# Optimization experiments

Hardware: AMD Instinct MI355X
Metric: run time of the kernel (lower is better)

## Reference

```python
import jax, jax.numpy as jnp
import numpy as np

B, T, D, H = 32, 4096, 512, 512


def setup_inputs() -> dict:
    key = jax.random.key(0)
    ks = jax.random.split(key, 8)
    s = 1.0 / np.sqrt(D)
    return {
        "hidden_state": jax.random.normal(ks[0], (B, D), jnp.float32),
        "encoder_outputs": jax.random.normal(ks[1], (B, T, D), jnp.float32),
        "W": jax.random.normal(ks[2], (D, H), jnp.float32) * s,
        "U": jax.random.normal(ks[3], (D, H), jnp.float32) * s,
        "V": jax.random.normal(ks[4], (H,), jnp.float32) * s,
        "bias": jnp.zeros((H,), jnp.float32),
        "Wa": jax.random.normal(ks[5], (H, H), jnp.float32) * (1.0 / np.sqrt(H)),
        "ba": jnp.zeros((H,), jnp.float32),
    }


def reference(hidden_state, encoder_outputs, W, U, V, bias, Wa, ba):
    # dens1: [B,1,H] ; dens2: [B,T,H]
    dens1 = jnp.einsum('bd,dh->bh', hidden_state, W)[:, None, :]
    dens2 = jnp.einsum('btd,dh->bth', encoder_outputs, U)
    pre = dens1 + dens2 + bias                       # [B,T,H]
    tanh_ = jnp.tanh(jnp.einsum('bth,hk->btk', pre, Wa) + ba)  # extra Dense(tanh)
    cij = jnp.einsum('bth,h->bt', tanh_, V)          # [B,T]
    alphas = jax.nn.softmax(cij, axis=-1)            # [B,T]
    output = jnp.einsum('btd,bt->bd', encoder_outputs, alphas)  # weighted sum
    return output, alphas
```

## Files before the change

### kernel.cpp

```cpp
#include <hip/hip_runtime.h>
#include <hip/hip_bf16.h>


#define BB 32
#define TT 4096
#define DD 512
#define HH 512
#define BK 64

typedef short s16x8 __attribute__((ext_vector_type(8)));
typedef float f32x4 __attribute__((ext_vector_type(4)));

union FU { float f; unsigned u; };

static __device__ __forceinline__ unsigned pack_bf16_trunc(float a, float b) {
    FU ua, ub; ua.f = a; ub.f = b;
    return (ua.u >> 16) | (ub.u & 0xffff0000u);
}

static __device__ __forceinline__ unsigned short f2bf_rne(float x) {
    FU v; v.f = x;
    unsigned u = v.u;
    u = u + 0x7fffu + ((u >> 16) & 1u);
    return (unsigned short)(u >> 16);
}

static __device__ __forceinline__ float tanh_fast(float x) {
    float e = __expf(2.0f * x);
    return 1.0f - 2.0f * __builtin_amdgcn_rcpf(e + 1.0f);
}

static __device__ __forceinline__ void gload_lds16(const void* g, void* l) {
    __builtin_amdgcn_global_load_lds(
        (const __attribute__((address_space(1))) unsigned int*)g,
        (__attribute__((address_space(3))) unsigned int*)l, 16, 0, 0);
}

__global__ void k_prep(const float* __restrict__ hs, const float* __restrict__ W,
                       const float* __restrict__ bias, const float* __restrict__ Wa,
                       const float* __restrict__ ba, const float* __restrict__ U,
                       float* __restrict__ cvec, unsigned short* __restrict__ UWaT) {
    int bi = blockIdx.x;
    int tid = threadIdx.x;
    __shared__ float sm[8 * DD];
    if (bi < 32) {
        int b = bi;
        float* hsb = sm;
        float* gs = sm + DD;
        hsb[tid] = hs[b * DD + tid];
        hsb[tid + 256] = hs[b * DD + tid + 256];
        __syncthreads();
        float a0 = bias[tid], a1 = bias[tid + 256];
        #pragma unroll 4
        for (int d = 0; d < DD; ++d) {
            float h = hsb[d];
            a0 = fmaf(h, W[(size_t)d * HH + tid], a0);
            a1 = fmaf(h, W[(size_t)d * HH + tid + 256], a1);
        }
        gs[tid] = a0;
        gs[tid + 256] = a1;
        __syncthreads();
        float c0 = ba[tid], c1 = ba[tid + 256];
        #pragma unroll 4
        for (int h = 0; h < HH; ++h) {
            float g = gs[h];
            c0 = fmaf(g, Wa[(size_t)h * HH + tid], c0);
            c1 = fmaf(g, Wa[(size_t)h * HH + tid + 256], c1);
        }
        cvec[b * HH + tid] = c0;
        cvec[b * HH + tid + 256] = c1;
    } else {
        int d0 = (bi - 32) * 8;
        float (*Us)[DD] = (float (*)[DD])sm;
        #pragma unroll
        for (int i = 0; i < 16; ++i) {
            int idx = i * 256 + tid;
            Us[idx >> 9][idx & 511] = U[(size_t)(d0 + (idx >> 9)) * HH + (idx & 511)];
        }
        __syncthreads();
        float acc[8][2] = {};
        #pragma unroll 2
        for (int h = 0; h < DD; ++h) {
            float w0 = Wa[(size_t)h * HH + tid];
            float w1 = Wa[(size_t)h * HH + 256 + tid];
            #pragma unroll
            for (int dd = 0; dd < 8; ++dd) {
                float u = Us[dd][h];
                acc[dd][0] = fmaf(u, w0, acc[dd][0]);
                acc[dd][1] = fmaf(u, w1, acc[dd][1]);
            }
        }
        #pragma unroll
        for (int dd = 0; dd < 8; ++dd) {
            UWaT[(size_t)tid * DD + d0 + dd] = f2bf_rne(acc[dd][0]);
            UWaT[(size_t)(tid + 256) * DD + d0 + dd] = f2bf_rne(acc[dd][1]);
        }
    }
}

__global__ void __launch_bounds__(256, 2) k_gemm_tanh(
    const float* __restrict__ e, const unsigned short* __restrict__ Bt,
    const float* __restrict__ cvec, const float* __restrict__ V,
    float* __restrict__ cij) {
    int tid = threadIdx.x;
    int m0 = blockIdx.x * 64;
    int lane = tid & 63, w = tid >> 6;
    int wn = w * 128;
    int lcol = lane & 15, q = lane >> 4;
    int rl = lane >> 3, gg = lane & 7;

    __shared__ __align__(16) unsigned short As[64 * BK];
    __shared__ __align__(16) unsigned short Bs[512 * BK];

    f32x4 acc[4][8] = {};

    int arow[4], ac4[4];
    #pragma unroll
    for (int it = 0; it < 4; ++it) {
        int idx = it * 256 + tid;
        arow[it] = idx >> 4;
        ac4[it] = idx & 15;
    }
    const float* Abase = e + (size_t)m0 * DD;

    float4 av[4];
    #pragma unroll
    for (int it = 0; it < 4; ++it)
        av[it] = *(const float4*)(Abase + (size_t)arow[it] * DD + ac4[it] * 4);

    for (int k0 = 0; k0 < DD; k0 += BK) {
        if (k0) __syncthreads();
        #pragma unroll
        for (int u = 0; u < 16; ++u) {
            int n0 = w * 128 + u * 8;
            const unsigned short* gp =
                Bt + (size_t)(n0 + rl) * DD + k0 + ((gg ^ rl) << 3);
            gload_lds16(gp, &Bs[n0 * 64]);
        }
        #pragma unroll
        for (int it = 0; it < 4; ++it) {
            uint2 wv;
            wv.x = pack_bf16_trunc(av[it].x, av[it].y);
            wv.y = pack_bf16_trunc(av[it].z, av[it].w);
            int g = ac4[it] >> 1, half = ac4[it] & 1;
            *(uint2*)&As[(g * 64 + (arow[it] ^ g)) * 8 + half * 4] = wv;
        }
        __syncthreads();
        if (k0 < DD - BK) {
            #pragma unroll
            for (int it = 0; it < 4; ++it)
                av[it] = *(const float4*)(Abase + (size_t)arow[it] * DD +
                                          (k0 + BK) + ac4[it] * 4);
        }
        #pragma unroll
        for (int ks = 0; ks < BK; ks += 32) {
            int gk = ks >> 3;
            s16x8 af[4], bfr[8];
            #pragma unroll
            for (int i = 0; i < 4; ++i) {
                int row = i * 16 + lcol, g = gk + q;
                af[i] = *(const s16x8*)&As[(g * 64 + (row ^ g)) * 8];
            }
            #pragma unroll
            for (int j = 0; j < 8; ++j) {
                int col = wn + j * 16 + lcol, g = gk + q;
                bfr[j] = *(const s16x8*)&Bs[col * 64 + ((g ^ (col & 7)) << 3)];
            }
            #pragma unroll
            for (int i = 0; i < 4; ++i)
                #pragma unroll
                for (int j = 0; j < 8; ++j)
                    acc[i][j] = __builtin_amdgcn_mfma_f32_16x16x32_bf16(
                        af[i], bfr[j], acc[i][j], 0, 0, 0);
        }
    }

    __syncthreads();
    float* red = (float*)As;
    int b = m0 >> 12;
    float cvv[8], Vv[8];
    #pragma unroll
    for (int j = 0; j < 8; ++j) {
        int h = wn + j * 16 + lcol;
        cvv[j] = cvec[b * HH + h];
        Vv[j] = V[h];
    }
    #pragma unroll
    for (int i = 0; i < 4; ++i) {
        #pragma unroll
        for (int r = 0; r < 4; ++r) {
            float s = 0.0f;
            #pragma unroll
            for (int j = 0; j < 8; ++j)
                s = fmaf(tanh_fast(acc[i][j][r] + cvv[j]), Vv[j], s);
            s += __shfl_xor(s, 1);
            s += __shfl_xor(s, 2);
            s += __shfl_xor(s, 4);
            s += __shfl_xor(s, 8);
            if (lcol == 0)
                red[w * 64 + i * 16 + q * 4 + r] = s;
        }
    }
    __syncthreads();
    if (tid < 64)
        cij[m0 + tid] = red[tid] + red[64 + tid] + red[128 + tid] + red[192 + tid];
}

__global__ void k_softmax(const float* __restrict__ cij, float* __restrict__ alphas) {
    int b = blockIdx.x, tid = threadIdx.x;
    const float* row = cij + (size_t)b * TT;
    __shared__ float red[4];
    float m = -1e30f;
    for (int t = tid; t < TT; t += 256) m = fmaxf(m, row[t]);
    #pragma unroll
    for (int o = 1; o < 64; o <<= 1) m = fmaxf(m, __shfl_xor(m, o));
    if ((tid & 63) == 0) red[tid >> 6] = m;
    __syncthreads();
    m = fmaxf(fmaxf(red[0], red[1]), fmaxf(red[2], red[3]));
    __syncthreads();
    float sum = 0.0f;
    for (int t = tid; t < TT; t += 256) sum += __expf(row[t] - m);
    #pragma unroll
    for (int o = 1; o < 64; o <<= 1) sum += __shfl_xor(sum, o);
    if ((tid & 63) == 0) red[tid >> 6] = sum;
    __syncthreads();
    float inv = 1.0f / (red[0] + red[1] + red[2] + red[3]);
    for (int t = tid; t < TT; t += 256)
        alphas[(size_t)b * TT + t] = __expf(row[t] - m) * inv;
}

__global__ void k_wsum(const float* __restrict__ e, const float* __restrict__ alphas,
                       float* __restrict__ pw) {
    int b = blockIdx.x >> 6;
    int chunk = blockIdx.x & 63;
    int tid = threadIdx.x;
    int half = tid >> 7, f4 = tid & 127;
    const float* base = e + (size_t)b * TT * DD + (size_t)chunk * 64 * DD + f4 * 4;
    const float* al = alphas + (size_t)b * TT + chunk * 64;
    f32x4 a0 = {0,0,0,0}, a1 = {0,0,0,0}, a2 = {0,0,0,0}, a3 = {0,0,0,0};
    for (int it = 0; it < 8; ++it) {
        int t = it * 8 + half;
        float w0 = al[t], w1 = al[t + 2], w2 = al[t + 4], w3 = al[t + 6];
        a0 += w0 * *(const f32x4*)(base + (size_t)t * DD);
        a1 += w1 * *(const f32x4*)(base + (size_t)(t + 2) * DD);
        a2 += w2 * *(const f32x4*)(base + (size_t)(t + 4) * DD);
        a3 += w3 * *(const f32x4*)(base + (size_t)(t + 6) * DD);
    }
    a0 += a1; a2 += a3; a0 += a2;
    __shared__ f32x4 red[128];
    if (half == 1) red[f4] = a0;
    __syncthreads();
    if (half == 0) {
        a0 += red[f4];
        *(f32x4*)&pw[((size_t)(b * 64 + chunk)) * DD + f4 * 4] = a0;
    }
}

__global__ void k_wred(const float* __restrict__ pw, float* __restrict__ out) {
    int b = blockIdx.x, tid = threadIdx.x;
    float2 acc = {0.0f, 0.0f};
    const float* base = pw + (size_t)b * 64 * DD;
    #pragma unroll 4
    for (int c = 0; c < 64; ++c) {
        float2 v = *(const float2*)(base + (size_t)c * DD + tid * 2);
        acc.x += v.x;
        acc.y += v.y;
    }
    *(float2*)&out[b * DD + tid * 2] = acc;
}

extern "C" void kernel_launch(void* const* d_in, const int* in_sizes, int n_in,
                              void* d_out, int out_size, void* d_ws, size_t ws_size,
                              hipStream_t stream) {
    const float* hs   = (const float*)d_in[0];
    const float* e    = (const float*)d_in[1];
    const float* W    = (const float*)d_in[2];
    const float* U    = (const float*)d_in[3];
    const float* V    = (const float*)d_in[4];
    const float* bias = (const float*)d_in[5];
    const float* Wa   = (const float*)d_in[6];
    const float* ba   = (const float*)d_in[7];

    float* out    = (float*)d_out;
    float* alphas = out + BB * DD;

    float*          cij  = (float*)d_ws;
    float*          cvec = (float*)((char*)d_ws + 524288);
    unsigned short* Bt   = (unsigned short*)((char*)d_ws + 589824);
    float*          pw   = (float*)((char*)d_ws + 1179648);


    k_prep<<<96, 256, 0, stream>>>(hs, W, bias, Wa, ba, U, cvec, Bt);
    k_gemm_tanh<<<2048, 256, 0, stream>>>(e, Bt, cvec, V, cij);
    k_softmax<<<BB, 256, 0, stream>>>(cij, alphas);
    k_wsum<<<BB * 64, 256, 0, stream>>>(e, alphas, pw);
    k_wred<<<BB, 256, 0, stream>>>(pw, out);
}
```

Before: 569.6 us.

## Pre-swizzle B into MFMA fragment layout and stage full A tile in LDS

The prep kernel now writes the fused U·Wa weight matrix in a fragment-major layout, so each lane of the GEMM kernel loads its B operand straight from global/L2 into registers with one 16-byte load. The B staging in LDS goes away, and those loads are double-buffered across the 16 k-steps. The whole 64x512 A tile is converted to bf16 and stored in LDS once up front, which removes the per-k-step barriers. In exchange, LDS use per block grows to 64KB for A and there is no prefetch of A overlapped with compute. The B operand is also re-read from L2 by every block instead of being shared through LDS.

```diff
diff --git a/kernel.cpp b/kernel.cpp
--- a/kernel.cpp
+++ b/kernel.cpp
@@ -6,7 +6,6 @@
 #define TT 4096
 #define DD 512
 #define HH 512
-#define BK 64
 
 typedef short s16x8 __attribute__((ext_vector_type(8)));
 typedef float f32x4 __attribute__((ext_vector_type(4)));
@@ -30,16 +29,10 @@
     return 1.0f - 2.0f * __builtin_amdgcn_rcpf(e + 1.0f);
 }
 
-static __device__ __forceinline__ void gload_lds16(const void* g, void* l) {
-    __builtin_amdgcn_global_load_lds(
-        (const __attribute__((address_space(1))) unsigned int*)g,
-        (__attribute__((address_space(3))) unsigned int*)l, 16, 0, 0);
-}
-
 __global__ void k_prep(const float* __restrict__ hs, const float* __restrict__ W,
                        const float* __restrict__ bias, const float* __restrict__ Wa,
                        const float* __restrict__ ba, const float* __restrict__ U,
-                       float* __restrict__ cvec, unsigned short* __restrict__ UWaT) {
+                       float* __restrict__ cvec, unsigned short* __restrict__ Btf) {
     int bi = blockIdx.x;
     int tid = threadIdx.x;
     __shared__ float sm[8 * DD];
@@ -90,16 +83,21 @@
                 acc[dd][1] = fmaf(u, w1, acc[dd][1]);
             }
         }
-        #pragma unroll
-        for (int dd = 0; dd < 8; ++dd) {
-            UWaT[(size_t)tid * DD + d0 + dd] = f2bf_rne(acc[dd][0]);
-            UWaT[(size_t)(tid + 256) * DD + d0 + dd] = f2bf_rne(acc[dd][1]);
+        int fk = d0 >> 5, qq = (d0 >> 3) & 3;
+        #pragma unroll
+        for (int half = 0; half < 2; ++half) {
+            int n = tid + half * 256;
+            unsigned short tmp[8];
+            #pragma unroll
+            for (int dd = 0; dd < 8; ++dd) tmp[dd] = f2bf_rne(acc[dd][half]);
+            size_t base = ((size_t)((n >> 4) * 16 + fk) * 64 + (n & 15) + (qq << 4)) * 8;
+            *(uint4*)&Btf[base] = *(const uint4*)tmp;
         }
     }
 }
 
 __global__ void __launch_bounds__(256, 2) k_gemm_tanh(
-    const float* __restrict__ e, const unsigned short* __restrict__ Bt,
+    const float* __restrict__ e, const unsigned short* __restrict__ Btf,
     const float* __restrict__ cvec, const float* __restrict__ V,
     float* __restrict__ cij) {
     int tid = threadIdx.x;
@@ -107,72 +105,54 @@
     int lane = tid & 63, w = tid >> 6;
     int wn = w * 128;
     int lcol = lane & 15, q = lane >> 4;
-    int rl = lane >> 3, gg = lane & 7;
-
-    __shared__ __align__(16) unsigned short As[64 * BK];
-    __shared__ __align__(16) unsigned short Bs[512 * BK];
-
+
+    __shared__ __align__(16) unsigned short As[64 * DD];
+
+    const float* Abase = e + (size_t)m0 * DD;
+    #pragma unroll
+    for (int it = 0; it < 16; ++it) {
+        int idx = it * 256 + tid;
+        int m = idx >> 6, c2 = idx & 63;
+        const float* p = Abase + (size_t)m * DD + c2 * 8;
+        float4 v0 = *(const float4*)p;
+        float4 v1 = *(const float4*)(p + 4);
+        uint4 u;
+        u.x = pack_bf16_trunc(v0.x, v0.y);
+        u.y = pack_bf16_trunc(v0.z, v0.w);
+        u.z = pack_bf16_trunc(v1.x, v1.y);
+        u.w = pack_bf16_trunc(v1.z, v1.w);
+        *(uint4*)&As[(m * 64 + (c2 ^ m)) * 8] = u;
+    }
+    __syncthreads();
+
+    const unsigned short* Bw = Btf + (size_t)(w * 8) * 16 * 64 * 8;
     f32x4 acc[4][8] = {};
-
-    int arow[4], ac4[4];
-    #pragma unroll
-    for (int it = 0; it < 4; ++it) {
-        int idx = it * 256 + tid;
-        arow[it] = idx >> 4;
-        ac4[it] = idx & 15;
-    }
-    const float* Abase = e + (size_t)m0 * DD;
-
-    float4 av[4];
-    #pragma unroll
-    for (int it = 0; it < 4; ++it)
-        av[it] = *(const float4*)(Abase + (size_t)arow[it] * DD + ac4[it] * 4);
-
-    for (int k0 = 0; k0 < DD; k0 += BK) {
-        if (k0) __syncthreads();
-        #pragma unroll
-        for (int u = 0; u < 16; ++u) {
-            int n0 = w * 128 + u * 8;
-            const unsigned short* gp =
-                Bt + (size_t)(n0 + rl) * DD + k0 + ((gg ^ rl) << 3);
-            gload_lds16(gp, &Bs[n0 * 64]);
-        }
-        #pragma unroll
-        for (int it = 0; it < 4; ++it) {
-            uint2 wv;
-            wv.x = pack_bf16_trunc(av[it].x, av[it].y);
-            wv.y = pack_bf16_trunc(av[it].z, av[it].w);
-            int g = ac4[it] >> 1, half = ac4[it] & 1;
-            *(uint2*)&As[(g * 64 + (arow[it] ^ g)) * 8 + half * 4] = wv;
-        }
-        __syncthreads();
-        if (k0 < DD - BK) {
-            #pragma unroll
-            for (int it = 0; it < 4; ++it)
-                av[it] = *(const float4*)(Abase + (size_t)arow[it] * DD +
-                                          (k0 + BK) + ac4[it] * 4);
-        }
-        #pragma unroll
-        for (int ks = 0; ks < BK; ks += 32) {
-            int gk = ks >> 3;
-            s16x8 af[4], bfr[8];
-            #pragma unroll
-            for (int i = 0; i < 4; ++i) {
-                int row = i * 16 + lcol, g = gk + q;
-                af[i] = *(const s16x8*)&As[(g * 64 + (row ^ g)) * 8];
-            }
-            #pragma unroll
-            for (int j = 0; j < 8; ++j) {
-                int col = wn + j * 16 + lcol, g = gk + q;
-                bfr[j] = *(const s16x8*)&Bs[col * 64 + ((g ^ (col & 7)) << 3)];
-            }
-            #pragma unroll
-            for (int i = 0; i < 4; ++i)
-                #pragma unroll
-                for (int j = 0; j < 8; ++j)
-                    acc[i][j] = __builtin_amdgcn_mfma_f32_16x16x32_bf16(
-                        af[i], bfr[j], acc[i][j], 0, 0, 0);
-        }
+    s16x8 bfr[2][8];
+    #pragma unroll
+    for (int j = 0; j < 8; ++j)
+        bfr[0][j] = *(const s16x8*)(Bw + ((size_t)(j * 16 + 0) * 64 + lane) * 8);
+
+    #pragma unroll
+    for (int kk = 0; kk < 16; ++kk) {
+        int cur = kk & 1;
+        if (kk < 15) {
+            #pragma unroll
+            for (int j = 0; j < 8; ++j)
+                bfr[cur ^ 1][j] =
+                    *(const s16x8*)(Bw + ((size_t)(j * 16 + kk + 1) * 64 + lane) * 8);
+        }
+        s16x8 af[4];
+        #pragma unroll
+        for (int i = 0; i < 4; ++i) {
+            int m = i * 16 + lcol;
+            af[i] = *(const s16x8*)&As[(m * 64 + ((kk * 4 + q) ^ m)) * 8];
+        }
+        #pragma unroll
+        for (int i = 0; i < 4; ++i)
+            #pragma unroll
+            for (int j = 0; j < 8; ++j)
+                acc[i][j] = __builtin_amdgcn_mfma_f32_16x16x32_bf16(
+                    af[i], bfr[cur][j], acc[i][j], 0, 0, 0);
     }
 
     __syncthreads();
@@ -286,12 +266,12 @@
 
     float*          cij  = (float*)d_ws;
     float*          cvec = (float*)((char*)d_ws + 524288);
-    unsigned short* Bt   = (unsigned short*)((char*)d_ws + 589824);
+    unsigned short* Btf  = (unsigned short*)((char*)d_ws + 589824);
     float*          pw   = (float*)((char*)d_ws + 1179648);
 
 
-    k_prep<<<96, 256, 0, stream>>>(hs, W, bias, Wa, ba, U, cvec, Bt);
-    k_gemm_tanh<<<2048, 256, 0, stream>>>(e, Bt, cvec, V, cij);
+    k_prep<<<96, 256, 0, stream>>>(hs, W, bias, Wa, ba, U, cvec, Btf);
+    k_gemm_tanh<<<2048, 256, 0, stream>>>(e, Btf, cvec, V, cij);
     k_softmax<<<BB, 256, 0, stream>>>(cij, alphas);
     k_wsum<<<BB * 64, 256, 0, stream>>>(e, alphas, pw);
     k_wred<<<BB, 256, 0, stream>>>(pw, out);
```

New measurement: 574.3 us. Within noise of the previous version (+0.8%).
